# Kernel optimization log

Measured on AMD Instinct MI355X. Metric: run time of the kernel, lower is better.

## Reference

```python
import jax, jax.numpy as jnp
import numpy as np

V, E, H, L = 37, 256, 512, 3
B, S = 512, 128


def lstm_layer(x, W_ih, W_hh, b_ih, b_hh):
    # x: [B,S,D_in]; W_ih: [4H,D_in]; W_hh: [4H,H]; PyTorch gate order i,f,g,o
    Bx = x.shape[0]
    Hh = W_hh.shape[1]
    x_proj = jnp.einsum('bsd,gd->bsg', x, W_ih) + b_ih + b_hh  # [B,S,4H]

    def step(carry, xt):
        h, c = carry
        gates = xt + h @ W_hh.T
        i, f, g, o = jnp.split(gates, 4, axis=-1)
        i = jax.nn.sigmoid(i)
        f = jax.nn.sigmoid(f)
        g = jnp.tanh(g)
        o = jax.nn.sigmoid(o)
        c = f * c + i * g
        h = o * jnp.tanh(c)
        return (h, c), h

    init = (jnp.zeros((Bx, Hh), x.dtype), jnp.zeros((Bx, Hh), x.dtype))
    (hT, cT), hs = jax.lax.scan(step, init, jnp.swapaxes(x_proj, 0, 1))
    return jnp.swapaxes(hs, 0, 1), hT, cT


def setup_inputs() -> dict:
    key = jax.random.key(0)
    ks = jax.random.split(key, 16)
    inp = {'tokens': jax.random.randint(ks[0], (B, S), 0, V)}
    inp['embedding'] = jax.random.normal(ks[1], (V, E), jnp.float32) * 0.05
    for l in range(L):
        d_in = E if l == 0 else H
        inp[f'W_ih{l}'] = jax.random.normal(ks[2 + 4 * l], (4 * H, d_in), jnp.float32) * 0.05
        inp[f'W_hh{l}'] = jax.random.normal(ks[3 + 4 * l], (4 * H, H), jnp.float32) * 0.05
        inp[f'b_ih{l}'] = jnp.zeros((4 * H,), jnp.float32)
        inp[f'b_hh{l}'] = jnp.zeros((4 * H,), jnp.float32)
    inp['W_out'] = jax.random.normal(ks[14], (V, H), jnp.float32) * 0.05
    inp['b_out'] = jnp.zeros((V,), jnp.float32)
    return inp


def reference(tokens, embedding, W_ih0, W_hh0, b_ih0, b_hh0,
              W_ih1, W_hh1, b_ih1, b_hh1,
              W_ih2, W_hh2, b_ih2, b_hh2, W_out, b_out):
    x = embedding[tokens]  # [B,S,E]
    hs, cs = [], []
    for (Wi, Wh, bi, bh) in ((W_ih0, W_hh0, b_ih0, b_hh0),
                             (W_ih1, W_hh1, b_ih1, b_hh1),
                             (W_ih2, W_hh2, b_ih2, b_hh2)):
        x, hT, cT = lstm_layer(x, Wi, Wh, bi, bh)
        hs.append(hT)
        cs.append(cT)
    logits = jnp.einsum('bsh,vh->bsv', x, W_out) + b_out  # [B,S,V]
    return logits, jnp.stack(hs), jnp.stack(cs)
```

## Files before the change

kernel.cpp:

```cpp
#include <hip/hip_runtime.h>

typedef __attribute__((ext_vector_type(4))) float f32x4;
typedef __attribute__((ext_vector_type(8))) short bf16x8;

#define DEV __device__ __forceinline__

DEV float b2f(ushort u) { return __uint_as_float(((uint)u) << 16); }
DEV ushort f2b(float f) {
    uint u = __float_as_uint(f);
    return (ushort)((u + 0x7fffu + ((u >> 16) & 1u)) >> 16);
}
DEV float fsig(float x) {
    return __builtin_amdgcn_rcpf(1.f + __builtin_amdgcn_exp2f(-1.4426950408889634f * x));
}
DEV float ftanh(float x) {
    return 1.f - 2.f * __builtin_amdgcn_rcpf(__builtin_amdgcn_exp2f(2.885390081777927f * x) + 1.f);
}
DEV void gload_lds16(const void* g, void* l) {
    __builtin_amdgcn_global_load_lds(
        (const __attribute__((address_space(1))) void*)g,
        (__attribute__((address_space(3))) void*)l, 16, 0, 0);
}
DEV void gload_lds16_l2(const void* g, void* l) {
    __builtin_amdgcn_global_load_lds(
        (const __attribute__((address_space(1))) void*)g,
        (__attribute__((address_space(3))) void*)l, 16, 0, 1);
}
DEV void store_l2_u32(uint* p, uint v) {
    asm volatile("global_store_dword %0, %1, off sc0" :: "v"(p), "v"(v) : "memory");
}
DEV void store_sc_u32(uint* p, uint v) {
    asm volatile("global_store_dword %0, %1, off sc0 sc1" :: "v"(p), "v"(v) : "memory");
}
DEV uint load_l2_u32(const uint* p) {
    uint v;
    asm volatile("global_load_dword %0, %1, off sc0\n\ts_waitcnt vmcnt(0)"
                 : "=v"(v) : "v"(p) : "memory");
    return v;
}
DEV uint load_sc_u32(const uint* p) {
    uint v;
    asm volatile("global_load_dword %0, %1, off sc0 sc1\n\ts_waitcnt vmcnt(0)"
                 : "=v"(v) : "v"(p) : "memory");
    return v;
}

__global__ void f2b_kernel(const float* __restrict__ s, ushort* __restrict__ d, int n) {
    int i = blockIdx.x * 256 + threadIdx.x;
    if (i < n) d[i] = f2b(s[i]);
}

__global__ __launch_bounds__(256) void embed_kernel(
    const int* __restrict__ tok, const float* __restrict__ emb, ushort* __restrict__ x0) {
    const int nthr = gridDim.x * 256;
    for (int idx = blockIdx.x * 256 + threadIdx.x; idx < 128 * 512 * 32; idx += nthr) {
        const int row = idx >> 5;
        const int g8 = idx & 31;
        const int t = row >> 9, b = row & 511;
        const int tk = tok[b * 128 + t];
        const float* ep = emb + (size_t)tk * 256 + g8 * 8;
        float4 a = *(const float4*)ep;
        float4 c = *(const float4*)(ep + 4);
        uint4 o;
        o.x = (uint)f2b(a.x) | ((uint)f2b(a.y) << 16);
        o.y = (uint)f2b(a.z) | ((uint)f2b(a.w) << 16);
        o.z = (uint)f2b(c.x) | ((uint)f2b(c.y) << 16);
        o.w = (uint)f2b(c.z) | ((uint)f2b(c.w) << 16);
        *(uint4*)(x0 + (size_t)row * 256 + g8 * 8) = o;
    }
}

__global__ __launch_bounds__(256) void gemm_bias_kernel(
    const ushort* __restrict__ A, const ushort* __restrict__ Bw,
    const float* __restrict__ bias0, const float* __restrict__ bias1,
    ushort* __restrict__ C, int M, int N, int K) {
    __shared__ ushort la[128 * 32];
    __shared__ ushort lb[128 * 32];
    const int tid = threadIdx.x;
    const int wave = tid >> 6, lane = tid & 63;
    const int ntn = N >> 7;
    const int tm = blockIdx.x / ntn, tn = blockIdx.x % ntn;
    const int m0 = tm << 7, n0 = tn << 7;
    const int wm = (wave >> 1) * 64, wn = (wave & 1) * 64;
    f32x4 acc[4][4] = {};
    const int nks = K >> 5;
    const int srow = tid >> 2, scol = (tid & 3) * 8;
    for (int ks = 0; ks < nks; ++ks) {
        const int k0 = ks << 5;
#pragma unroll
        for (int r = 0; r < 2; ++r) {
            gload_lds16(A + (size_t)(m0 + r * 64 + srow) * K + k0 + scol, &la[r * 2048 + wave * 512]);
            gload_lds16(Bw + (size_t)(n0 + r * 64 + srow) * K + k0 + scol, &lb[r * 2048 + wave * 512]);
        }
        __syncthreads();
        bf16x8 af[4], bfr[4];
#pragma unroll
        for (int i = 0; i < 4; ++i)
            af[i] = *(const bf16x8*)&la[(wm + i * 16 + (lane & 15)) * 32 + (lane >> 4) * 8];
#pragma unroll
        for (int i = 0; i < 4; ++i)
            bfr[i] = *(const bf16x8*)&lb[(wn + i * 16 + (lane & 15)) * 32 + (lane >> 4) * 8];
#pragma unroll
        for (int mi = 0; mi < 4; ++mi)
#pragma unroll
            for (int ni = 0; ni < 4; ++ni)
                acc[mi][ni] = __builtin_amdgcn_mfma_f32_16x16x32_bf16(af[mi], bfr[ni], acc[mi][ni], 0, 0, 0);
        __syncthreads();
    }
#pragma unroll
    for (int mi = 0; mi < 4; ++mi) {
        int row = m0 + wm + mi * 16 + ((lane >> 4) << 2);
#pragma unroll
        for (int j = 0; j < 4; ++j) {
#pragma unroll
            for (int ni = 0; ni < 4; ++ni) {
                int col = n0 + wn + ni * 16 + (lane & 15);
                C[(size_t)(row + j) * N + col] = f2b(acc[mi][ni][j] + bias0[col] + bias1[col]);
            }
        }
    }
}

__global__ __launch_bounds__(256) void lstm_chunk_kernel(
    const ushort* __restrict__ xpj,
    const ushort* __restrict__ Whh,
    ushort* __restrict__ hs,
    float* __restrict__ cstate,
    float* __restrict__ hT, float* __restrict__ cT,
    uint* __restrict__ bar,
    int t0) {
    __shared__ ushort hp[64 * 512];
    __shared__ float gbuf[4][64][20];
    const int tid = threadIdx.x;
    const int wave = tid >> 6, lane = tid & 63;
    const int grp = blockIdx.x & 7;
    const int hsl = blockIdx.x >> 3;
    const int b0 = grp << 6, h0 = hsl << 4;
    uint* gflags = bar + grp * 512;
    uint* myflag = gflags + hsl * 16;

    __threadfence();

    bf16x8 Bfr[16];
    const ushort* wb = Whh + ((size_t)(wave * 512 + h0 + (lane & 15))) * 512 + (lane >> 4) * 8;
#pragma unroll
    for (int ks = 0; ks < 16; ++ks) Bfr[ks] = *(const bf16x8*)(wb + ks * 32);

    float creg[4];
#pragma unroll
    for (int i = 0; i < 2; ++i) {
        const int e2 = i * 512 + tid * 2;
        const size_t ci = (size_t)(b0 + (e2 >> 4)) * 512 + h0 + (e2 & 15);
        if (t0 > 0) {
            float2 cv = *(const float2*)&cstate[ci];
            creg[2 * i] = cv.x; creg[2 * i + 1] = cv.y;
        } else {
            creg[2 * i] = 0.f; creg[2 * i + 1] = 0.f;
        }
    }

    uint xqc[8];
#pragma unroll
    for (int i = 0; i < 2; ++i) {
        const int e2 = i * 512 + tid * 2;
        const uint* xb = (const uint*)(xpj + (size_t)(b0 + (e2 >> 4)) * 2048 + h0 + (e2 & 15));
        xqc[i * 4 + 0] = xb[0]; xqc[i * 4 + 1] = xb[256];
        xqc[i * 4 + 2] = xb[512]; xqc[i * 4 + 3] = xb[768];
    }

    for (int tt = 0; tt < 32; ++tt) {
        const int t = t0 + tt;
        if (tt > 0) {
            if (wave == 0) {
                const uint* fp = gflags + ((lane & 31) << 4);
                const uint target = (uint)tt;
                int k = 0;
                for (;;) {
                    uint v = ((++k & 7) == 0) ? load_sc_u32(fp) : load_l2_u32(fp);
                    if (__all(v >= target)) break;
                    __builtin_amdgcn_s_sleep(1);
                }
            }
            __syncthreads();
        }
        f32x4 acc[4] = {};
        uint xqn[8];
        if (t > 0) {
            const ushort* hprev = hs + (size_t)(t - 1) * 262144;
#pragma unroll
            for (int rr = 0; rr < 16; ++rr) {
                const int row = rr * 4 + wave;
                gload_lds16_l2(hprev + (size_t)(b0 + row) * 512 + ((lane ^ (row & 7)) * 8),
                               &hp[row * 512]);
            }
            if (tt < 31) {
                const ushort* xt = xpj + (size_t)(tt + 1) * 1048576;
#pragma unroll
                for (int i = 0; i < 2; ++i) {
                    const int e2 = i * 512 + tid * 2;
                    const uint* xb = (const uint*)(xt + (size_t)(b0 + (e2 >> 4)) * 2048 + h0 + (e2 & 15));
                    xqn[i * 4 + 0] = xb[0]; xqn[i * 4 + 1] = xb[256];
                    xqn[i * 4 + 2] = xb[512]; xqn[i * 4 + 3] = xb[768];
                }
            }
            __syncthreads();
#pragma unroll
            for (int ks = 0; ks < 16; ++ks) {
#pragma unroll
                for (int mi = 0; mi < 4; ++mi) {
                    const int row = mi * 16 + (lane & 15);
                    const int c16 = (ks * 4 + (lane >> 4)) ^ (row & 7);
                    bf16x8 af = *(const bf16x8*)&hp[row * 512 + c16 * 8];
                    acc[mi] = __builtin_amdgcn_mfma_f32_16x16x32_bf16(af, Bfr[ks], acc[mi], 0, 0, 0);
                }
            }
        } else if (tt < 31) {
            const ushort* xt = xpj + (size_t)(tt + 1) * 1048576;
#pragma unroll
            for (int i = 0; i < 2; ++i) {
                const int e2 = i * 512 + tid * 2;
                const uint* xb = (const uint*)(xt + (size_t)(b0 + (e2 >> 4)) * 2048 + h0 + (e2 & 15));
                xqn[i * 4 + 0] = xb[0]; xqn[i * 4 + 1] = xb[256];
                xqn[i * 4 + 2] = xb[512]; xqn[i * 4 + 3] = xb[768];
            }
        }
#pragma unroll
        for (int mi = 0; mi < 4; ++mi) {
            const int rloc = mi * 16 + ((lane >> 4) << 2);
#pragma unroll
            for (int j = 0; j < 4; ++j) gbuf[wave][rloc + j][lane & 15] = acc[mi][j];
        }
        __syncthreads();
        ushort* hout = hs + (size_t)t * 262144;
#pragma unroll
        for (int i = 0; i < 2; ++i) {
            const int e2 = i * 512 + tid * 2;
            const int b = e2 >> 4, hh = e2 & 15;
            float2 gI = *(const float2*)&gbuf[0][b][hh];
            float2 gF = *(const float2*)&gbuf[1][b][hh];
            float2 gG = *(const float2*)&gbuf[2][b][hh];
            float2 gO = *(const float2*)&gbuf[3][b][hh];
            float i0 = fsig(gI.x + b2f((ushort)(xqc[i * 4 + 0] & 0xffff)));
            float i1 = fsig(gI.y + b2f((ushort)(xqc[i * 4 + 0] >> 16)));
            float f0 = fsig(gF.x + b2f((ushort)(xqc[i * 4 + 1] & 0xffff)));
            float f1 = fsig(gF.y + b2f((ushort)(xqc[i * 4 + 1] >> 16)));
            float g0 = ftanh(gG.x + b2f((ushort)(xqc[i * 4 + 2] & 0xffff)));
            float g1 = ftanh(gG.y + b2f((ushort)(xqc[i * 4 + 2] >> 16)));
            float o0 = fsig(gO.x + b2f((ushort)(xqc[i * 4 + 3] & 0xffff)));
            float o1 = fsig(gO.y + b2f((ushort)(xqc[i * 4 + 3] >> 16)));
            float c0 = f0 * creg[2 * i] + i0 * g0;
            float c1 = f1 * creg[2 * i + 1] + i1 * g1;
            float h0v = o0 * ftanh(c0);
            float h1v = o1 * ftanh(c1);
            creg[2 * i] = c0; creg[2 * i + 1] = c1;
            const size_t ci = (size_t)(b0 + b) * 512 + h0 + hh;
            store_l2_u32((uint*)(hout + ci), (uint)f2b(h0v) | ((uint)f2b(h1v) << 16));
            if (t == 127) {
                *(float2*)&hT[ci] = make_float2(h0v, h1v);
                *(float2*)&cT[ci] = make_float2(c0, c1);
            }
        }
        if (tt < 31) {
#pragma unroll
            for (int k = 0; k < 8; ++k) xqc[k] = xqn[k];
            asm volatile("s_waitcnt vmcnt(0)" ::: "memory");
            __syncthreads();
            if (tid == 0) {
                store_l2_u32(myflag, (uint)(tt + 1));
                store_sc_u32(myflag, (uint)(tt + 1));
            }
        }
    }
#pragma unroll
    for (int i = 0; i < 2; ++i) {
        const int e2 = i * 512 + tid * 2;
        const size_t ci = (size_t)(b0 + (e2 >> 4)) * 512 + h0 + (e2 & 15);
        *(float2*)&cstate[ci] = make_float2(creg[2 * i], creg[2 * i + 1]);
    }
}

__global__ __launch_bounds__(256) void outproj_kernel(
    const ushort* __restrict__ hs, const float* __restrict__ Wout,
    const float* __restrict__ bout, float* __restrict__ out) {
    __shared__ ushort lh[32 * 512];
    const int tid = threadIdx.x;
    const size_t r0 = (size_t)blockIdx.x * 32;
    const uint4* gs = (const uint4*)(hs + r0 * 512);
    uint4* ls = (uint4*)lh;
    for (int i = tid; i < 2048; i += 256) ls[i] = gs[i];
    __syncthreads();
    const int rg = tid & 7, vg = tid >> 3;
    float acc[4][2] = {};
    for (int k8 = 0; k8 < 64; ++k8) {
        float hf[4][8];
#pragma unroll
        for (int rr = 0; rr < 4; ++rr) {
            bf16x8 hv = *(const bf16x8*)&lh[(rg * 4 + rr) * 512 + k8 * 8];
#pragma unroll
            for (int j = 0; j < 8; ++j) hf[rr][j] = b2f((ushort)hv[j]);
        }
#pragma unroll
        for (int vi = 0; vi < 2; ++vi) {
            int v = vg + vi * 32;
            if (v < 37) {
                const float* wp = Wout + (size_t)v * 512 + k8 * 8;
                float4 w0 = *(const float4*)wp;
                float4 w1 = *(const float4*)(wp + 4);
                float wv[8] = {w0.x, w0.y, w0.z, w0.w, w1.x, w1.y, w1.z, w1.w};
#pragma unroll
                for (int rr = 0; rr < 4; ++rr) {
                    float s = 0.f;
#pragma unroll
                    for (int j = 0; j < 8; ++j) s += hf[rr][j] * wv[j];
                    acc[rr][vi] += s;
                }
            }
        }
    }
#pragma unroll
    for (int vi = 0; vi < 2; ++vi) {
        int v = vg + vi * 32;
        if (v < 37) {
#pragma unroll
            for (int rr = 0; rr < 4; ++rr) {
                size_t r = r0 + rg * 4 + rr;
                int t = (int)(r >> 9), b = (int)(r & 511);
                out[((size_t)b * 128 + t) * 37 + v] = acc[rr][vi] + bout[v];
            }
        }
    }
}

extern "C" void kernel_launch(void* const* d_in, const int* in_sizes, int n_in,
                              void* d_out, int out_size, void* d_ws, size_t ws_size,
                              hipStream_t stream) {
    (void)in_sizes; (void)n_in; (void)out_size; (void)ws_size;
    const int* tokens = (const int*)d_in[0];
    const float* emb = (const float*)d_in[1];
    const float* Wih_f[3] = {(const float*)d_in[2], (const float*)d_in[6], (const float*)d_in[10]};
    const float* Whh_f[3] = {(const float*)d_in[3], (const float*)d_in[7], (const float*)d_in[11]};
    const float* bih[3] = {(const float*)d_in[4], (const float*)d_in[8], (const float*)d_in[12]};
    const float* bhh[3] = {(const float*)d_in[5], (const float*)d_in[9], (const float*)d_in[13]};
    const float* Wout = (const float*)d_in[14];
    const float* bout = (const float*)d_in[15];
    float* out = (float*)d_out;

    char* ws = (char*)d_ws;
    size_t off = 0;
    auto take = [&](size_t nb) -> void* {
        void* p = ws + off;
        off = (off + nb + 255) & ~(size_t)255;
        return p;
    };
    ushort* x0 = (ushort*)take((size_t)128 * 512 * 256 * 2);
    ushort* hsA = (ushort*)take((size_t)128 * 512 * 512 * 2);
    ushort* hsB = (ushort*)take((size_t)128 * 512 * 512 * 2);
    ushort* xpj = (ushort*)take((size_t)32 * 512 * 2048 * 2);
    float* cst = (float*)take((size_t)512 * 512 * 4);
    ushort* wih[3];
    wih[0] = (ushort*)take((size_t)2048 * 256 * 2);
    wih[1] = (ushort*)take((size_t)2048 * 512 * 2);
    wih[2] = (ushort*)take((size_t)2048 * 512 * 2);
    ushort* whh[3];
    for (int l = 0; l < 3; ++l) whh[l] = (ushort*)take((size_t)2048 * 512 * 2);
    uint* barbase = (uint*)take((size_t)12 * 4096 * 4);

    hipMemsetAsync(barbase, 0, (size_t)12 * 4096 * 4, stream);

    f2b_kernel<<<2048, 256, 0, stream>>>(Wih_f[0], wih[0], 2048 * 256);
    f2b_kernel<<<4096, 256, 0, stream>>>(Wih_f[1], wih[1], 2048 * 512);
    f2b_kernel<<<4096, 256, 0, stream>>>(Wih_f[2], wih[2], 2048 * 512);
    for (int l = 0; l < 3; ++l)
        f2b_kernel<<<4096, 256, 0, stream>>>(Whh_f[l], whh[l], 2048 * 512);

    embed_kernel<<<2048, 256, 0, stream>>>(tokens, emb, x0);

    float* hTbase = out + 2424832;
    float* cTbase = out + 2424832 + 786432;
    const ushort* src = x0;
    ushort* hs_out = hsA;
    for (int l = 0; l < 3; ++l) {
        int K = (l == 0) ? 256 : 512;
        hs_out = (l == 1) ? hsB : hsA;
        for (int ch = 0; ch < 4; ++ch) {
            gemm_bias_kernel<<<2048, 256, 0, stream>>>(
                src + (size_t)ch * 16384 * K, wih[l], bih[l], bhh[l], xpj, 16384, 2048, K);
            lstm_chunk_kernel<<<256, 256, 0, stream>>>(
                xpj, whh[l], hs_out, cst,
                hTbase + (size_t)l * 262144, cTbase + (size_t)l * 262144,
                barbase + (size_t)(l * 4 + ch) * 4096, ch * 32);
        }
        src = hs_out;
    }
    outproj_kernel<<<2048, 256, 0, stream>>>(hs_out, Wout, bout, out);
}
```

Before: 2.810 ms.

## Wavefront-pipeline LSTM layers in 16-step chunks, running two cells concurrently

The sequence is split into 8 chunks of 16 steps per layer, and a wavefront schedule runs the recurrence of two (layer, chunk) cells in one launch of 512 blocks. The input-projection GEMMs for both cells are likewise fused into one launch. Layers can now overlap instead of running strictly one after another, which fills more of the GPU than 256 blocks did. Per-layer h histories become ring buffers of three slots, and the spin wait drops the cheaper L2-only polling so every load and store uses sc0 sc1. The costs are twice as many grid-barrier waits per step count, more launches, and a possible deadlock if not all 512 blocks are co-resident.

```diff
diff --git a/kernel.cpp b/kernel.cpp
--- a/kernel.cpp
+++ b/kernel.cpp
@@ -26,17 +26,8 @@
         (const __attribute__((address_space(1))) void*)g,
         (__attribute__((address_space(3))) void*)l, 16, 0, 1);
 }
-DEV void store_l2_u32(uint* p, uint v) {
-    asm volatile("global_store_dword %0, %1, off sc0" :: "v"(p), "v"(v) : "memory");
-}
 DEV void store_sc_u32(uint* p, uint v) {
     asm volatile("global_store_dword %0, %1, off sc0 sc1" :: "v"(p), "v"(v) : "memory");
-}
-DEV uint load_l2_u32(const uint* p) {
-    uint v;
-    asm volatile("global_load_dword %0, %1, off sc0\n\ts_waitcnt vmcnt(0)"
-                 : "=v"(v) : "v"(p) : "memory");
-    return v;
 }
 DEV uint load_sc_u32(const uint* p) {
     uint v;
@@ -70,16 +61,24 @@
     }
 }
 
-__global__ __launch_bounds__(256) void gemm_bias_kernel(
-    const ushort* __restrict__ A, const ushort* __restrict__ Bw,
-    const float* __restrict__ bias0, const float* __restrict__ bias1,
-    ushort* __restrict__ C, int M, int N, int K) {
+struct GemmSet { const ushort* A; const ushort* Bw; const float* b0; const float* b1;
+                 ushort* C; int K; };
+__global__ __launch_bounds__(256) void gemm_pair_kernel(
+    const ushort* A0, const ushort* B0, const float* b00, const float* b01, ushort* C0, int K0,
+    const ushort* A1, const ushort* B1, const float* b10, const float* b11, ushort* C1, int K1) {
     __shared__ ushort la[128 * 32];
     __shared__ ushort lb[128 * 32];
     const int tid = threadIdx.x;
     const int wave = tid >> 6, lane = tid & 63;
-    const int ntn = N >> 7;
-    const int tm = blockIdx.x / ntn, tn = blockIdx.x % ntn;
+    const int sel = blockIdx.x >> 10;
+    const int tile = blockIdx.x & 1023;
+    const ushort* A = sel ? A1 : A0;
+    const ushort* Bw = sel ? B1 : B0;
+    const float* bias0 = sel ? b10 : b00;
+    const float* bias1 = sel ? b11 : b01;
+    ushort* C = sel ? C1 : C0;
+    const int K = sel ? K1 : K0;
+    const int tm = tile >> 4, tn = tile & 15;
     const int m0 = tm << 7, n0 = tn << 7;
     const int wm = (wave >> 1) * 64, wn = (wave & 1) * 64;
     f32x4 acc[4][4] = {};
@@ -115,26 +114,24 @@
 #pragma unroll
             for (int ni = 0; ni < 4; ++ni) {
                 int col = n0 + wn + ni * 16 + (lane & 15);
-                C[(size_t)(row + j) * N + col] = f2b(acc[mi][ni][j] + bias0[col] + bias1[col]);
-            }
-        }
-    }
-}
-
-__global__ __launch_bounds__(256) void lstm_chunk_kernel(
-    const ushort* __restrict__ xpj,
-    const ushort* __restrict__ Whh,
-    ushort* __restrict__ hs,
-    float* __restrict__ cstate,
-    float* __restrict__ hT, float* __restrict__ cT,
-    uint* __restrict__ bar,
-    int t0) {
-    __shared__ ushort hp[64 * 512];
-    __shared__ float gbuf[4][64][20];
-    const int tid = threadIdx.x;
+                C[(size_t)(row + j) * 2048 + col] = f2b(acc[mi][ni][j] + bias0[col] + bias1[col]);
+            }
+        }
+    }
+}
+
+struct RecSM { ushort hp[64 * 512]; float gbuf[4][64][16]; };
+
+DEV void rec_cell(RecSM& sm,
+                  const ushort* __restrict__ xpj,
+                  const ushort* __restrict__ Whh,
+                  ushort* __restrict__ cur,
+                  const ushort* __restrict__ prev,
+                  float* __restrict__ cst, float* __restrict__ hT, float* __restrict__ cT,
+                  uint* __restrict__ bar, int ch, int bid, int tid) {
     const int wave = tid >> 6, lane = tid & 63;
-    const int grp = blockIdx.x & 7;
-    const int hsl = blockIdx.x >> 3;
+    const int grp = bid & 7;
+    const int hsl = bid >> 3;
     const int b0 = grp << 6, h0 = hsl << 4;
     uint* gflags = bar + grp * 512;
     uint* myflag = gflags + hsl * 16;
@@ -151,8 +148,8 @@
     for (int i = 0; i < 2; ++i) {
         const int e2 = i * 512 + tid * 2;
         const size_t ci = (size_t)(b0 + (e2 >> 4)) * 512 + h0 + (e2 & 15);
-        if (t0 > 0) {
-            float2 cv = *(const float2*)&cstate[ci];
+        if (ch > 0) {
+            float2 cv = *(const float2*)&cst[ci];
             creg[2 * i] = cv.x; creg[2 * i + 1] = cv.y;
         } else {
             creg[2 * i] = 0.f; creg[2 * i + 1] = 0.f;
@@ -168,32 +165,27 @@
         xqc[i * 4 + 2] = xb[512]; xqc[i * 4 + 3] = xb[768];
     }
 
-    for (int tt = 0; tt < 32; ++tt) {
-        const int t = t0 + tt;
+    for (int tt = 0; tt < 16; ++tt) {
+        const int t = ch * 16 + tt;
         if (tt > 0) {
             if (wave == 0) {
                 const uint* fp = gflags + ((lane & 31) << 4);
                 const uint target = (uint)tt;
-                int k = 0;
-                for (;;) {
-                    uint v = ((++k & 7) == 0) ? load_sc_u32(fp) : load_l2_u32(fp);
-                    if (__all(v >= target)) break;
-                    __builtin_amdgcn_s_sleep(1);
-                }
+                while (!__all(load_sc_u32(fp) >= target)) __builtin_amdgcn_s_sleep(1);
             }
             __syncthreads();
         }
         f32x4 acc[4] = {};
         uint xqn[8];
         if (t > 0) {
-            const ushort* hprev = hs + (size_t)(t - 1) * 262144;
+            const ushort* hprev = (tt > 0) ? (cur + (size_t)(tt - 1) * 262144) : prev;
 #pragma unroll
             for (int rr = 0; rr < 16; ++rr) {
                 const int row = rr * 4 + wave;
                 gload_lds16_l2(hprev + (size_t)(b0 + row) * 512 + ((lane ^ (row & 7)) * 8),
-                               &hp[row * 512]);
-            }
-            if (tt < 31) {
+                               &sm.hp[row * 512]);
+            }
+            if (tt < 15) {
                 const ushort* xt = xpj + (size_t)(tt + 1) * 1048576;
 #pragma unroll
                 for (int i = 0; i < 2; ++i) {
@@ -210,11 +202,11 @@
                 for (int mi = 0; mi < 4; ++mi) {
                     const int row = mi * 16 + (lane & 15);
                     const int c16 = (ks * 4 + (lane >> 4)) ^ (row & 7);
-                    bf16x8 af = *(const bf16x8*)&hp[row * 512 + c16 * 8];
+                    bf16x8 af = *(const bf16x8*)&sm.hp[row * 512 + c16 * 8];
                     acc[mi] = __builtin_amdgcn_mfma_f32_16x16x32_bf16(af, Bfr[ks], acc[mi], 0, 0, 0);
                 }
             }
-        } else if (tt < 31) {
+        } else if (tt < 15) {
             const ushort* xt = xpj + (size_t)(tt + 1) * 1048576;
 #pragma unroll
             for (int i = 0; i < 2; ++i) {
@@ -228,18 +220,18 @@
         for (int mi = 0; mi < 4; ++mi) {
             const int rloc = mi * 16 + ((lane >> 4) << 2);
 #pragma unroll
-            for (int j = 0; j < 4; ++j) gbuf[wave][rloc + j][lane & 15] = acc[mi][j];
+            for (int j = 0; j < 4; ++j) sm.gbuf[wave][rloc + j][lane & 15] = acc[mi][j];
         }
         __syncthreads();
-        ushort* hout = hs + (size_t)t * 262144;
+        ushort* hout = cur + (size_t)tt * 262144;
 #pragma unroll
         for (int i = 0; i < 2; ++i) {
             const int e2 = i * 512 + tid * 2;
             const int b = e2 >> 4, hh = e2 & 15;
-            float2 gI = *(const float2*)&gbuf[0][b][hh];
-            float2 gF = *(const float2*)&gbuf[1][b][hh];
-            float2 gG = *(const float2*)&gbuf[2][b][hh];
-            float2 gO = *(const float2*)&gbuf[3][b][hh];
+            float2 gI = *(const float2*)&sm.gbuf[0][b][hh];
+            float2 gF = *(const float2*)&sm.gbuf[1][b][hh];
+            float2 gG = *(const float2*)&sm.gbuf[2][b][hh];
+            float2 gO = *(const float2*)&sm.gbuf[3][b][hh];
             float i0 = fsig(gI.x + b2f((ushort)(xqc[i * 4 + 0] & 0xffff)));
             float i1 = fsig(gI.y + b2f((ushort)(xqc[i * 4 + 0] >> 16)));
             float f0 = fsig(gF.x + b2f((ushort)(xqc[i * 4 + 1] & 0xffff)));
@@ -254,28 +246,39 @@
             float h1v = o1 * ftanh(c1);
             creg[2 * i] = c0; creg[2 * i + 1] = c1;
             const size_t ci = (size_t)(b0 + b) * 512 + h0 + hh;
-            store_l2_u32((uint*)(hout + ci), (uint)f2b(h0v) | ((uint)f2b(h1v) << 16));
+            store_sc_u32((uint*)(hout + ci), (uint)f2b(h0v) | ((uint)f2b(h1v) << 16));
             if (t == 127) {
                 *(float2*)&hT[ci] = make_float2(h0v, h1v);
                 *(float2*)&cT[ci] = make_float2(c0, c1);
             }
         }
-        if (tt < 31) {
+        if (tt < 15) {
 #pragma unroll
             for (int k = 0; k < 8; ++k) xqc[k] = xqn[k];
             asm volatile("s_waitcnt vmcnt(0)" ::: "memory");
             __syncthreads();
-            if (tid == 0) {
-                store_l2_u32(myflag, (uint)(tt + 1));
-                store_sc_u32(myflag, (uint)(tt + 1));
-            }
+            if (tid == 0) store_sc_u32(myflag, (uint)(tt + 1));
         }
     }
 #pragma unroll
     for (int i = 0; i < 2; ++i) {
         const int e2 = i * 512 + tid * 2;
         const size_t ci = (size_t)(b0 + (e2 >> 4)) * 512 + h0 + (e2 & 15);
-        *(float2*)&cstate[ci] = make_float2(creg[2 * i], creg[2 * i + 1]);
+        *(float2*)&cst[ci] = make_float2(creg[2 * i], creg[2 * i + 1]);
+    }
+}
+
+__global__ __launch_bounds__(256) void fused_pair_kernel(
+    const ushort* xpjA, const ushort* WhhA, ushort* curA, const ushort* prevA,
+    float* cstA, float* hTA, float* cTA, uint* barA, int chA,
+    const ushort* xpjB, const ushort* WhhB, ushort* curB, const ushort* prevB,
+    float* cstB, float* hTB, float* cTB, uint* barB, int chB) {
+    __shared__ RecSM sm;
+    const int tid = threadIdx.x;
+    if (blockIdx.x < 256) {
+        rec_cell(sm, xpjA, WhhA, curA, prevA, cstA, hTA, cTA, barA, chA, blockIdx.x, tid);
+    } else {
+        rec_cell(sm, xpjB, WhhB, curB, prevB, cstB, hTB, cTB, barB, chB, blockIdx.x - 256, tid);
     }
 }
 
@@ -345,6 +348,7 @@
     const float* bout = (const float*)d_in[15];
     float* out = (float*)d_out;
 
+    const size_t SLOT = (size_t)16 * 512 * 512;
     char* ws = (char*)d_ws;
     size_t off = 0;
     auto take = [&](size_t nb) -> void* {
@@ -353,19 +357,22 @@
         return p;
     };
     ushort* x0 = (ushort*)take((size_t)128 * 512 * 256 * 2);
-    ushort* hsA = (ushort*)take((size_t)128 * 512 * 512 * 2);
-    ushort* hsB = (ushort*)take((size_t)128 * 512 * 512 * 2);
-    ushort* xpj = (ushort*)take((size_t)32 * 512 * 2048 * 2);
-    float* cst = (float*)take((size_t)512 * 512 * 4);
+    ushort* hsr0 = (ushort*)take(3 * SLOT * 2);
+    ushort* hsr1 = (ushort*)take(3 * SLOT * 2);
+    ushort* hs2 = (ushort*)take(8 * SLOT * 2);
+    ushort* xpjA = (ushort*)take((size_t)16 * 512 * 2048 * 2);
+    ushort* xpjB = (ushort*)take((size_t)16 * 512 * 2048 * 2);
+    float* cstL[3];
+    for (int l = 0; l < 3; ++l) cstL[l] = (float*)take((size_t)512 * 512 * 4);
     ushort* wih[3];
     wih[0] = (ushort*)take((size_t)2048 * 256 * 2);
     wih[1] = (ushort*)take((size_t)2048 * 512 * 2);
     wih[2] = (ushort*)take((size_t)2048 * 512 * 2);
     ushort* whh[3];
     for (int l = 0; l < 3; ++l) whh[l] = (ushort*)take((size_t)2048 * 512 * 2);
-    uint* barbase = (uint*)take((size_t)12 * 4096 * 4);
-
-    hipMemsetAsync(barbase, 0, (size_t)12 * 4096 * 4, stream);
+    uint* barbase = (uint*)take((size_t)24 * 4096 * 4);
+
+    hipMemsetAsync(barbase, 0, (size_t)24 * 4096 * 4, stream);
 
     f2b_kernel<<<2048, 256, 0, stream>>>(Wih_f[0], wih[0], 2048 * 256);
     f2b_kernel<<<4096, 256, 0, stream>>>(Wih_f[1], wih[1], 2048 * 512);
@@ -377,20 +384,52 @@
 
     float* hTbase = out + 2424832;
     float* cTbase = out + 2424832 + 786432;
-    const ushort* src = x0;
-    ushort* hs_out = hsA;
-    for (int l = 0; l < 3; ++l) {
-        int K = (l == 0) ? 256 : 512;
-        hs_out = (l == 1) ? hsB : hsA;
-        for (int ch = 0; ch < 4; ++ch) {
-            gemm_bias_kernel<<<2048, 256, 0, stream>>>(
-                src + (size_t)ch * 16384 * K, wih[l], bih[l], bhh[l], xpj, 16384, 2048, K);
-            lstm_chunk_kernel<<<256, 256, 0, stream>>>(
-                xpj, whh[l], hs_out, cst,
-                hTbase + (size_t)l * 262144, cTbase + (size_t)l * 262144,
-                barbase + (size_t)(l * 4 + ch) * 4096, ch * 32);
-        }
-        src = hs_out;
-    }
-    outproj_kernel<<<2048, 256, 0, stream>>>(hs_out, Wout, bout, out);
-}
+
+    auto cell_cur = [&](int l, int c) -> ushort* {
+        if (l == 0) return hsr0 + (size_t)(c % 3) * SLOT;
+        if (l == 1) return hsr1 + (size_t)(c % 3) * SLOT;
+        return hs2 + (size_t)c * SLOT;
+    };
+    auto cell_prev = [&](int l, int c) -> const ushort* {
+        if (c == 0) return (const ushort*)nullptr;
+        if (l == 0) return hsr0 + (size_t)((c - 1) % 3) * SLOT + (size_t)15 * 262144;
+        if (l == 1) return hsr1 + (size_t)((c - 1) % 3) * SLOT + (size_t)15 * 262144;
+        return hs2 + (size_t)(c - 1) * SLOT + (size_t)15 * 262144;
+    };
+    auto gemm_A = [&](int l, int c) -> const ushort* {
+        if (l == 0) return x0 + (size_t)c * 8192 * 256;
+        return (l == 1 ? hsr0 : hsr1) + (size_t)(c % 3) * SLOT;
+    };
+
+    const int WV[14][2] = {{0, -1}, {1, 8},  {2, 9},  {3, 16}, {4, 10},  {11, 17}, {5, 12},
+                           {6, 18}, {13, 19}, {7, 14}, {15, 20}, {21, -1}, {22, -1}, {23, -1}};
+
+    for (int w = 0; w < 14; ++w) {
+        const int idA = WV[w][0], idB = WV[w][1];
+        const int lA = idA / 8, cA = idA % 8;
+        if (idB >= 0) {
+            const int lB = idB / 8, cB = idB % 8;
+            gemm_pair_kernel<<<2048, 256, 0, stream>>>(
+                gemm_A(lA, cA), wih[lA], bih[lA], bhh[lA], xpjA, (lA == 0) ? 256 : 512,
+                gemm_A(lB, cB), wih[lB], bih[lB], bhh[lB], xpjB, (lB == 0) ? 256 : 512);
+            fused_pair_kernel<<<512, 256, 0, stream>>>(
+                xpjA, whh[lA], cell_cur(lA, cA), cell_prev(lA, cA), cstL[lA],
+                hTbase + (size_t)lA * 262144, cTbase + (size_t)lA * 262144,
+                barbase + (size_t)idA * 4096, cA,
+                xpjB, whh[lB], cell_cur(lB, cB), cell_prev(lB, cB), cstL[lB],
+                hTbase + (size_t)lB * 262144, cTbase + (size_t)lB * 262144,
+                barbase + (size_t)idB * 4096, cB);
+        } else {
+            gemm_pair_kernel<<<1024, 256, 0, stream>>>(
+                gemm_A(lA, cA), wih[lA], bih[lA], bhh[lA], xpjA, (lA == 0) ? 256 : 512,
+                nullptr, nullptr, nullptr, nullptr, nullptr, 512);
+            fused_pair_kernel<<<256, 256, 0, stream>>>(
+                xpjA, whh[lA], cell_cur(lA, cA), cell_prev(lA, cA), cstL[lA],
+                hTbase + (size_t)lA * 262144, cTbase + (size_t)lA * 262144,
+                barbase + (size_t)idA * 4096, cA,
+                nullptr, nullptr, nullptr, nullptr, nullptr, nullptr, nullptr, nullptr, 0);
+        }
+    }
+
+    outproj_kernel<<<2048, 256, 0, stream>>>(hs2, Wout, bout, out);
+}
```

After: 3.875 ms. 1.38x slower.
